# Performance work log

Hardware: AMD Instinct MI355X
Metric: run time of the kernel (lower is better)

## Reference

```python
import jax, jax.numpy as jnp
import numpy as np

N, D, K = 65536, 256, 4096
INIT_COUNT = 100  # torch: counts = ones(K, int32) * 100


def setup_inputs() -> dict:
    key = jax.random.key(0)
    k1, k2 = jax.random.split(key)
    embedded = jax.random.normal(k1, (N, D), dtype=jnp.float32)
    centers = jax.random.normal(k2, (K, D), dtype=jnp.float32)
    counts = jnp.full((K,), INIT_COUNT, dtype=jnp.int32)
    return {"embedded": embedded, "centers": centers, "counts": counts}


def reference(embedded, centers, counts):
    # --- predict_hard: squared euclidean distance [N,K] + argmin ---
    x2 = jnp.sum(embedded * embedded, axis=1, keepdims=True)       # [N,1]
    c2 = jnp.sum(centers * centers, axis=1)                        # [K]
    d2 = x2 - 2.0 * (embedded @ centers.T) + c2                    # [N,K]
    labels = jnp.argmin(d2, axis=1).astype(jnp.int32)              # [N]

    # --- dcn_loss: mean over batch of squared dist to assigned center ---
    loss = jnp.sum((embedded - centers[labels]) ** 2) / embedded.shape[0]

    # --- update_centroids: sequential running-mean update, closed form ---
    # c <- (1-1/n)c + (1/n)x repeated over assigned samples collapses to
    # (count0 * c0 + sum_assigned x) / (count0 + m)
    seg_sum = jax.ops.segment_sum(embedded, labels, num_segments=K)            # [K,D]
    seg_cnt = jax.ops.segment_sum(
        jnp.ones((embedded.shape[0],), dtype=embedded.dtype), labels, num_segments=K
    )                                                                           # [K]
    c0 = counts.astype(embedded.dtype)                                          # [K]
    new_centers = (c0[:, None] * centers + seg_sum) / (c0 + seg_cnt)[:, None]  # [K,D]
    new_counts = counts + seg_cnt.astype(jnp.int32)                             # [K]
    return labels, new_centers, new_counts, loss
```

## Files before the change

kernel.cpp:

```cpp
#include <hip/hip_runtime.h>
#include <cfloat>
#include <cstdint>

constexpr int N  = 65536;
constexpr int D  = 256;
constexpr int K  = 4096;

typedef __attribute__((ext_vector_type(8))) _Float16 half8;
typedef __attribute__((ext_vector_type(8))) unsigned short ushort8;
typedef __attribute__((ext_vector_type(4))) float floatx4;

__device__ __forceinline__ floatx4 mfma_f16(half8 a, half8 b, floatx4 c) {
    return __builtin_amdgcn_mfma_f32_16x16x32_f16(a, b, c, 0, 0, 0);
}

__device__ __forceinline__ void ld_lds16(void* lds, const void* g) {
    __builtin_amdgcn_global_load_lds(
        (const __attribute__((address_space(1))) unsigned int*)g,
        (__attribute__((address_space(3))) unsigned int*)lds, 16, 0, 0);
}

__global__ void prep_c2(const float* __restrict__ C, float* __restrict__ c2) {
    int k = blockIdx.x;
    int l = threadIdx.x;
    const float4* row = (const float4*)(C + (size_t)k * D);
    float4 v = row[l];
    float s = v.x*v.x + v.y*v.y + v.z*v.z + v.w*v.w;
    #pragma unroll
    for (int m = 1; m < 64; m <<= 1) s += __shfl_xor(s, m);
    if (l == 0) c2[k] = s;
}

__global__ void convert_f16_both(const float* __restrict__ X, const float* __restrict__ C,
                                 unsigned short* __restrict__ Xh,
                                 unsigned short* __restrict__ Ch,
                                 float* __restrict__ xsq_part,
                                 float* __restrict__ c2) {
    __shared__ float red[4];
    int id = blockIdx.x * 256 + threadIdx.x;
    const int nX = N * D / 8;
    bool isX = id < nX;
    const float* src; unsigned short* dst;
    if (isX) { src = X; dst = Xh; }
    else     { src = C; dst = Ch; id -= nX; }
    const float4* s4 = (const float4*)src;
    float4 a = s4[2*id], b = s4[2*id+1];
    float xs[8] = {a.x,a.y,a.z,a.w,b.x,b.y,b.z,b.w};
    ushort8 h;
    float ps = 0.f;
    #pragma unroll
    for (int i = 0; i < 8; ++i) {
        union { _Float16 f; unsigned short u; } cv;
        cv.f = (_Float16)xs[i];
        h[i] = cv.u;
        ps += xs[i]*xs[i];
    }
    ((ushort8*)dst)[id] = h;
    int t = threadIdx.x;
    if (isX) {
        #pragma unroll
        for (int m = 1; m < 64; m <<= 1) ps += __shfl_xor(ps, m);
        if ((t & 63) == 0) red[t >> 6] = ps;
        __syncthreads();
        if (t == 0) xsq_part[blockIdx.x] = (red[0] + red[1]) + (red[2] + red[3]);
    } else {
        #pragma unroll
        for (int m = 1; m < 32; m <<= 1) ps += __shfl_xor(ps, m);
        if ((t & 31) == 0) c2[id >> 5] = ps;
    }
}

__global__ __launch_bounds__(256, 2) void mfma_assign(
        const unsigned short* __restrict__ Xh, const unsigned short* __restrict__ Ch,
        const float* __restrict__ c2, float* __restrict__ cand)
{
    __shared__ __align__(16) unsigned short sA[8*128*4*8];
    __shared__ __align__(16) unsigned short sB[2*128*4*8];

    const int t    = threadIdx.x;
    const int w    = t >> 6, l = t & 63;
    const int quad = l >> 4, lr = l & 15;
    const int wm   = w >> 1, wn = w & 1;
    const int rowbase = blockIdx.x * 128;
    const int kb   = blockIdx.y;

    const int rl  = l >> 2;
    const int gsw = (l & 3) ^ ((l >> 3) & 3);

    #pragma unroll
    for (int k = 0; k < 2; ++k) {
        int q = 2*w + k;
        const unsigned short* gp = Ch + (size_t)(kb*1024 + q*16 + rl)*D + gsw*8;
        ld_lds16((char*)sB + q*1024, gp);
    }
    #pragma unroll
    for (int k = 0; k < 16; ++k) {
        int q = w*16 + k;
        int c = q >> 3, rb = (q & 7) * 16;
        const unsigned short* gp = Xh + (size_t)(rowbase + rb + rl)*D + c*32 + gsw*8;
        ld_lds16((char*)sA + q*1024, gp);
    }

    const unsigned short* gpB = Ch + (size_t)(kb*1024 + 2*w*16 + rl)*D + gsw*8 + 32;

    const int sA_off = ((64*wm + lr)*4 + (quad ^ ((lr>>1)&3)))*16;
    const int sB_off = ((64*wn + lr)*4 + (quad ^ ((lr>>1)&3)))*16;

    float v1[16], v2[16]; int x1[16], x2s[16];
    #pragma unroll
    for (int i = 0; i < 16; ++i) { v1[i]=FLT_MAX; v2[i]=FLT_MAX; x1[i]=0x7fffffff; x2s[i]=0x7fffffff; }

    floatx4 acc[4][4];
    float c2v[4]; int jidx[4];
    int buf = 0;

    for (int chunk = 0; chunk < 64; ++chunk) {
        const int dk = chunk & 7;
        const int ct = kb*8 + (chunk >> 3);

        if (dk == 0) {
            #pragma unroll
            for (int i = 0; i < 4; ++i)
                #pragma unroll
                for (int j = 0; j < 4; ++j) acc[i][j] = (floatx4)0.f;
            const int colbase = ct*128 + 64*wn;
            #pragma unroll
            for (int j = 0; j < 4; ++j) {
                int col = colbase + 16*j + lr;
                c2v[j] = c2[col]; jidx[j] = col;
            }
        }

        __syncthreads();

        if (chunk < 63) {
            int nc = chunk + 1;
            ld_lds16((char*)sB + (buf^1)*8192 + (2*w+0)*1024, gpB);
            ld_lds16((char*)sB + (buf^1)*8192 + (2*w+1)*1024, gpB + 16*D);
            gpB += ((nc & 7) == 7) ? (size_t)(128*D - 7*32) : 32;
        }

        half8 Af[4], Bf[4];
        #pragma unroll
        for (int i = 0; i < 4; ++i)
            Af[i] = *(const half8*)((const char*)sA + dk*8192 + i*1024 + sA_off);
        #pragma unroll
        for (int j = 0; j < 4; ++j)
            Bf[j] = *(const half8*)((const char*)sB + buf*8192 + j*1024 + sB_off);
        #pragma unroll
        for (int j = 0; j < 4; ++j)
            #pragma unroll
            for (int i = 0; i < 4; ++i)
                acc[i][j] = mfma_f16(Af[i], Bf[j], acc[i][j]);

        if (dk == 7) {
            #pragma unroll
            for (int i = 0; i < 4; ++i)
                #pragma unroll
                for (int j = 0; j < 4; ++j)
                    #pragma unroll
                    for (int r = 0; r < 4; ++r) {
                        float s = fmaf(-2.f, acc[i][j][r], c2v[j]);
                        int st = 4*i + r;
                        bool cA = s < v1[st];
                        bool cB = s < v2[st];
                        float tv = cB ? s : v2[st]; int tx = cB ? jidx[j] : x2s[st];
                        v2[st] = cA ? v1[st] : tv;  x2s[st] = cA ? x1[st] : tx;
                        v1[st] = cA ? s : v1[st];   x1[st]  = cA ? jidx[j] : x1[st];
                    }
        }
        buf ^= 1;
    }

    #pragma unroll
    for (int i = 0; i < 4; ++i)
        #pragma unroll
        for (int r = 0; r < 4; ++r) {
            int st = 4*i + r;
            float a1 = v1[st], a2 = v2[st]; int ax1 = x1[st], ax2 = x2s[st];
            #pragma unroll
            for (int m = 1; m < 16; m <<= 1) {
                float b1f = __shfl_xor(a1, m); int bx1 = __shfl_xor(ax1, m);
                float b2f = __shfl_xor(a2, m); int bx2 = __shfl_xor(ax2, m);
                bool tt = (b1f < a1) || (b1f == a1 && bx1 < ax1);
                float n1 = tt ? b1f : a1; int nx1 = tt ? bx1 : ax1;
                float w1 = tt ? a1 : b1f; int wx1 = tt ? ax1 : bx1;
                float w2 = tt ? b2f : a2; int wx2 = tt ? bx2 : ax2;
                bool uu = (w2 < w1) || (w2 == w1 && wx2 < wx1);
                a1 = n1; ax1 = nx1;
                a2 = uu ? w2 : w1; ax2 = uu ? wx2 : wx1;
            }
            if (lr == 0) {
                int row = rowbase + 64*wm + 16*i + 4*quad + r;
                float4 o; o.x = a1; o.y = __int_as_float(ax1);
                o.z = a2; o.w = __int_as_float(ax2);
                ((float4*)cand)[(size_t)row*8 + 2*kb + wn] = o;
            }
        }
}

__global__ __launch_bounds__(256) void recheck_label(
        const float* __restrict__ X, const float* __restrict__ C,
        const float* __restrict__ c2, const float* __restrict__ cand,
        float* __restrict__ out_labels, int* __restrict__ labInt,
        int* __restrict__ cnt)
{
    int t = threadIdx.x, w = t >> 6, l = t & 63;
    int g  = l >> 4;
    int lr = l & 15;
    int row0 = (blockIdx.x * 4 + w) * 4;
    int row  = row0 + g;

    float4 e = ((const float4*)cand)[(size_t)row*8 + (lr >> 1)];
    float s  = (lr & 1) ? e.z : e.x;
    int  idx = (lr & 1) ? __float_as_int(e.w) : __float_as_int(e.y);

    float a1 = s, a2 = FLT_MAX; int ax1 = idx, ax2 = 0x7fffffff;
    #pragma unroll
    for (int m = 1; m < 16; m <<= 1) {
        float b1 = __shfl_xor(a1, m); int bx1 = __shfl_xor(ax1, m);
        float b2 = __shfl_xor(a2, m); int bx2 = __shfl_xor(ax2, m);
        bool tt = (b1 < a1) || (b1 == a1 && bx1 < ax1);
        float n1 = tt ? b1 : a1; int nx1 = tt ? bx1 : ax1;
        float w1 = tt ? a1 : b1; int wx1 = tt ? ax1 : bx1;
        float w2 = tt ? b2 : a2; int wx2 = tt ? bx2 : ax2;
        bool uu = (w2 < w1) || (w2 == w1 && wx2 < wx1);
        a1 = n1; ax1 = nx1;
        a2 = uu ? w2 : w1; ax2 = uu ? wx2 : wx1;
    }

    bool certain = (a2 - a1 > 0.25f);
    unsigned long long certMask = __ballot(certain);

    if (certain && lr == 0) {
        out_labels[row] = (float)ax1;
        labInt[row] = ax1;
        atomicAdd(&cnt[ax1], 1);
    }

    #pragma unroll
    for (int q = 0; q < 4; ++q) {
        if ((certMask >> (q*16)) & 1ull) continue;
        int r = row0 + q;
        float sq  = __shfl(s,   q*16 + lr);
        int   iq  = __shfl(idx, q*16 + lr);
        float gs1 = __shfl(a1,  q*16);

        float4 xv = ((const float4*)X)[(size_t)r*64 + l];
        float px = xv.x*xv.x + xv.y*xv.y + xv.z*xv.z + xv.w*xv.w;
        #pragma unroll
        for (int m = 1; m < 64; m <<= 1) px += __shfl_xor(px, m);

        bool active = (l < 16) && (sq <= gs1 + 0.25f);
        unsigned long long mask = __ballot(active);
        float best = FLT_MAX; int bi = 0x7fffffff;
        while (mask) {
            int k = __ffsll((long long)mask) - 1;
            mask &= mask - 1;
            int ck = __shfl(iq, k);
            float4 cv = ((const float4*)C)[(size_t)ck*64 + l];
            float pd = xv.x*cv.x + xv.y*cv.y + xv.z*cv.z + xv.w*cv.w;
            #pragma unroll
            for (int m = 1; m < 64; m <<= 1) pd += __shfl_xor(pd, m);
            float d2 = fmaf(-2.f, pd, px) + c2[ck];
            if (d2 < best || (d2 == best && ck < bi)) { best = d2; bi = ck; }
        }
        if (l == 0) {
            out_labels[r] = (float)bi;
            labInt[r] = bi;
            atomicAdd(&cnt[bi], 1);
        }
    }
}

__global__ void prefix_kernel(const int* __restrict__ cnt,
                              int* __restrict__ offs, int* __restrict__ cursor) {
    int l = threadIdx.x;
    int s = 0;
    #pragma unroll 8
    for (int i = 0; i < 64; ++i) s += cnt[l*64 + i];
    int inc = s;
    #pragma unroll
    for (int off = 1; off < 64; off <<= 1) {
        int u = __shfl_up(inc, off);
        if (l >= off) inc += u;
    }
    int run = inc - s;
    for (int i = 0; i < 64; ++i) {
        int k = l*64 + i;
        offs[k] = run; cursor[k] = run;
        run += cnt[k];
    }
}

__global__ void scatter_idx(const int* __restrict__ labInt,
                            int* __restrict__ cursor, int* __restrict__ sortedIdx) {
    int i = blockIdx.x * 256 + threadIdx.x;
    int lab = labInt[i];
    int pos = atomicAdd(&cursor[lab], 1);
    sortedIdx[pos] = i;
}

__global__ __launch_bounds__(256) void center_update(
        const float* __restrict__ X, const float* __restrict__ C,
        const int* __restrict__ counts0, const int* __restrict__ cnt,
        const int* __restrict__ offs, const int* __restrict__ sortedIdx,
        float* __restrict__ lossC, float* __restrict__ out)
{
    __shared__ float red[4];
    int k = blockIdx.x, d = threadIdx.x;
    int start = offs[k], m = cnt[k];
    float acc = 0.f;
    int i = 0;
    for (; i + 4 <= m; i += 4) {
        int r0 = sortedIdx[start+i],   r1 = sortedIdx[start+i+1];
        int r2 = sortedIdx[start+i+2], r3 = sortedIdx[start+i+3];
        float a0 = X[(size_t)r0*D + d], a1 = X[(size_t)r1*D + d];
        float a2 = X[(size_t)r2*D + d], a3 = X[(size_t)r3*D + d];
        acc += (a0 + a1) + (a2 + a3);
    }
    for (; i < m; ++i) acc += X[(size_t)sortedIdx[start+i]*D + d];

    float cv = C[(size_t)k*D + d];
    float c0 = (float)counts0[k];
    out[N + (size_t)k*D + d] = (c0 * cv + acc) / (c0 + (float)m);
    if (d == 0) out[N + (size_t)K*D + k] = (float)(counts0[k] + m);

    float lp = cv * fmaf((float)m, cv, -2.f*acc);
    #pragma unroll
    for (int s = 1; s < 64; s <<= 1) lp += __shfl_xor(lp, s);
    if ((d & 63) == 0) red[d >> 6] = lp;
    __syncthreads();
    if (d == 0) lossC[k] = (red[0] + red[1]) + (red[2] + red[3]);
}

__global__ __launch_bounds__(256) void loss_final(
        const float* __restrict__ xsq_part, const float* __restrict__ lossC,
        float* __restrict__ out)
{
    __shared__ double red[4];
    int t = threadIdx.x;
    double s = 0.0;
    for (int i = t; i < 8192; i += 256) s += (double)xsq_part[i];
    for (int i = t; i < 4096; i += 256) s += (double)lossC[i];
    #pragma unroll
    for (int m = 1; m < 64; m <<= 1) s += __shfl_xor(s, m);
    if ((t & 63) == 0) red[t >> 6] = s;
    __syncthreads();
    if (t == 0)
        out[N + (size_t)K*D + K] = (float)(((red[0] + red[1]) + (red[2] + red[3])) / (double)N);
}

__global__ void finalize_kernel(const float* __restrict__ C,
                                const int* __restrict__ counts0,
                                const float* __restrict__ seg,
                                const int* __restrict__ cnt,
                                const double* __restrict__ lossAcc,
                                float* __restrict__ out)
{
    int g = blockIdx.x * 256 + threadIdx.x;
    int k = g >> 8;
    float c0 = (float)counts0[k];
    float m  = (float)cnt[k];
    out[N + g] = (c0 * C[g] + seg[g]) / (c0 + m);
    if (g < K) out[N + (size_t)K*D + g] = (float)(counts0[g] + cnt[g]);
    if (g == 0) out[N + (size_t)K*D + K] = (float)(lossAcc[0] / (double)N);
}

__global__ __launch_bounds__(256, 2) void assign_fp32(
        const float* __restrict__ X, const float* __restrict__ C,
        const float* __restrict__ c2, float* __restrict__ out_labels,
        float* __restrict__ seg, int* __restrict__ cnt,
        double* __restrict__ lossAcc)
{
    constexpr int BM = 128, BN = 128, KD = 16;
    __shared__ float As[KD][BM];
    __shared__ float Bs[KD][BN];
    __shared__ float x2f[BM];
    __shared__ int   labs[BM];

    const int t  = threadIdx.x;
    const int tx = t & 15;
    const int ty = t >> 4;
    const int rowbase = blockIdx.x * BM;

    {
        int r  = t >> 1;
        int dh = (t & 1) * (D / 2);
        const float4* xr = (const float4*)(X + (size_t)(rowbase + r) * D + dh);
        float s = 0.f;
        #pragma unroll
        for (int i = 0; i < D / 8; ++i) {
            float4 v = xr[i];
            s += v.x*v.x + v.y*v.y + v.z*v.z + v.w*v.w;
        }
        s += __shfl_xor(s, 1);
        if ((t & 1) == 0) x2f[r] = s;
    }
    __syncthreads();

    float x2v[8];
    #pragma unroll
    for (int i = 0; i < 4; ++i) { x2v[i] = x2f[4*ty + i]; x2v[i+4] = x2f[64 + 4*ty + i]; }

    float rmv[8]; int rmi[8];
    #pragma unroll
    for (int i = 0; i < 8; ++i) { rmv[i] = FLT_MAX; rmi[i] = 0x7fffffff; }

    for (int ct = 0; ct < K / BN; ++ct) {
        float acc[8][8];
        #pragma unroll
        for (int i = 0; i < 8; ++i)
            #pragma unroll
            for (int j = 0; j < 8; ++j) acc[i][j] = 0.f;

        float c2f2[8];
        {
            float4 a = *(const float4*)(c2 + ct*BN + 4*tx);
            float4 b = *(const float4*)(c2 + ct*BN + 64 + 4*tx);
            c2f2[0]=a.x; c2f2[1]=a.y; c2f2[2]=a.z; c2f2[3]=a.w;
            c2f2[4]=b.x; c2f2[5]=b.y; c2f2[6]=b.z; c2f2[7]=b.w;
        }

        for (int dk = 0; dk < D / KD; ++dk) {
            #pragma unroll
            for (int i = 0; i < 2; ++i) {
                int f  = t + 256 * i;
                int r  = f >> 2;
                int dp = f & 3;
                float4 av = *(const float4*)(X + (size_t)(rowbase + r) * D + dk*KD + 4*dp);
                float4 bv = *(const float4*)(C + (size_t)(ct*BN + r) * D + dk*KD + 4*dp);
                As[4*dp+0][r]=av.x; As[4*dp+1][r]=av.y; As[4*dp+2][r]=av.z; As[4*dp+3][r]=av.w;
                Bs[4*dp+0][r]=bv.x; Bs[4*dp+1][r]=bv.y; Bs[4*dp+2][r]=bv.z; Bs[4*dp+3][r]=bv.w;
            }
            __syncthreads();
            #pragma unroll
            for (int kk = 0; kk < KD; ++kk) {
                float4 a0 = *(const float4*)&As[kk][4*ty];
                float4 a1 = *(const float4*)&As[kk][64 + 4*ty];
                float4 b0 = *(const float4*)&Bs[kk][4*tx];
                float4 b1 = *(const float4*)&Bs[kk][64 + 4*tx];
                float av[8] = {a0.x,a0.y,a0.z,a0.w,a1.x,a1.y,a1.z,a1.w};
                float bv[8] = {b0.x,b0.y,b0.z,b0.w,b1.x,b1.y,b1.z,b1.w};
                #pragma unroll
                for (int i = 0; i < 8; ++i)
                    #pragma unroll
                    for (int j = 0; j < 8; ++j)
                        acc[i][j] = fmaf(av[i], bv[j], acc[i][j]);
            }
            __syncthreads();
        }

        #pragma unroll
        for (int i = 0; i < 8; ++i) {
            float bv = FLT_MAX; int bi = 0x7fffffff;
            #pragma unroll
            for (int j = 0; j < 8; ++j) {
                int coll = (j < 4) ? (4*tx + j) : (64 + 4*tx + (j - 4));
                float v = fmaf(-2.f, acc[i][j], x2v[i]) + c2f2[j];
                int idx = ct * BN + coll;
                if (v < bv || (v == bv && idx < bi)) { bv = v; bi = idx; }
            }
            #pragma unroll
            for (int m = 1; m < 16; m <<= 1) {
                float ov = __shfl_xor(bv, m);
                int   oi = __shfl_xor(bi, m);
                if (ov < bv || (ov == bv && oi < bi)) { bv = ov; bi = oi; }
            }
            if (bv < rmv[i] || (bv == rmv[i] && bi < rmi[i])) { rmv[i] = bv; rmi[i] = bi; }
        }
    }

    if (tx == 0) {
        #pragma unroll
        for (int i = 0; i < 8; ++i) {
            int r = (i < 4) ? (4*ty + i) : (64 + 4*ty + (i - 4));
            labs[r] = rmi[i];
            out_labels[rowbase + r] = (float)rmi[i];
            atomicAdd(&cnt[rmi[i]], 1);
        }
    }
    __syncthreads();

    {
        int r   = t >> 1;
        int dh  = (t & 1) * (D / 2);
        int lab = labs[r];
        const float4* xr = (const float4*)(X + (size_t)(rowbase + r) * D + dh);
        const float4* cr = (const float4*)(C + (size_t)lab * D + dh);
        float* sp = seg + (size_t)lab * D + dh;
        float ls = 0.f;
        #pragma unroll 8
        for (int i = 0; i < D / 8; ++i) {
            float4 xv = xr[i];
            float4 cv = cr[i];
            atomicAdd(sp + 4*i + 0, xv.x);
            atomicAdd(sp + 4*i + 1, xv.y);
            atomicAdd(sp + 4*i + 2, xv.z);
            atomicAdd(sp + 4*i + 3, xv.w);
            float d0 = xv.x - cv.x, d1 = xv.y - cv.y;
            float d2 = xv.z - cv.z, d3 = xv.w - cv.w;
            ls += d0*d0 + d1*d1 + d2*d2 + d3*d3;
        }
        #pragma unroll
        for (int m = 1; m < 64; m <<= 1) ls += __shfl_xor(ls, m);
        if ((t & 63) == 0) atomicAdd(lossAcc, (double)ls);
    }
}

extern "C" void kernel_launch(void* const* d_in, const int* in_sizes, int n_in,
                              void* d_out, int out_size, void* d_ws, size_t ws_size,
                              hipStream_t stream) {
    const float* X       = (const float*)d_in[0];
    const float* C       = (const float*)d_in[1];
    const int*   counts0 = (const int*)d_in[2];
    float* out = (float*)d_out;

    char* p = (char*)d_ws;
    float*  seg     = (float*)p;          p += (size_t)K * D * 4;
    int*    cnt     = (int*)p;            p += (size_t)K * 4;
    float*  c2      = (float*)p;          p += (size_t)K * 4;
    double* lossAcc = (double*)p;         p += 16;
    size_t zero_all = (size_t)(p - (char*)d_ws);
    float*  cand    = (float*)p;          p += (size_t)N * 32 * 4;
    unsigned short* Xh = (unsigned short*)p; p += (size_t)N * D * 2;
    unsigned short* Ch = (unsigned short*)p; p += (size_t)K * D * 2;
    float* xsq_part = (float*)p;          p += 8192 * 4;
    float* lossC    = (float*)p;          p += (size_t)K * 4;
    size_t need = (size_t)(p - (char*)d_ws);

    int* labInt    = (int*)seg;
    int* sortedIdx = labInt + N;
    int* offs      = sortedIdx + N;
    int* cursor    = offs + K;

    if (ws_size >= need) {
        hipMemsetAsync(cnt, 0, (size_t)K * 4, stream);
        convert_f16_both<<<(N*D/8 + K*D/8)/256, 256, 0, stream>>>(X, C, Xh, Ch, xsq_part, c2);
        mfma_assign<<<dim3(N/128, 4), 256, 0, stream>>>(Xh, Ch, c2, cand);
        recheck_label<<<N/16, 256, 0, stream>>>(X, C, c2, cand, out, labInt, cnt);
        prefix_kernel<<<1, 64, 0, stream>>>(cnt, offs, cursor);
        scatter_idx<<<N/256, 256, 0, stream>>>(labInt, cursor, sortedIdx);
        center_update<<<K, 256, 0, stream>>>(X, C, counts0, cnt, offs, sortedIdx, lossC, out);
        loss_final<<<1, 256, 0, stream>>>(xsq_part, lossC, out);
    } else {
        hipMemsetAsync(d_ws, 0, zero_all, stream);
        prep_c2<<<K, 64, 0, stream>>>(C, c2);
        assign_fp32<<<N/128, 256, 0, stream>>>(X, C, c2, out, seg, cnt, lossAcc);
        finalize_kernel<<<(K*D)/256, 256, 0, stream>>>(C, counts0, seg, cnt, lossAcc, out);
    }
}
```

Before: 572.2 us.

## Pre-swizzle centers into MFMA fragment layout and load B directly from global

The f16 conversion kernel now writes the center matrix in a layout that matches the MFMA B-fragment order, so each lane can load its half8 operands straight from global/L2. The assign kernel drops the LDS double-buffer for B and the per-chunk __syncthreads, and instead software-pipelines register double-buffers for both A (from LDS) and B (from global) across the 8 K-slices. This removes barrier and LDS staging overhead in the distance GEMM. The cost is that B is re-read from L2 by each wave without LDS sharing, plus higher register pressure.

```diff
diff --git a/kernel.cpp b/kernel.cpp
--- a/kernel.cpp
+++ b/kernel.cpp
@@ -33,16 +33,16 @@
 
 __global__ void convert_f16_both(const float* __restrict__ X, const float* __restrict__ C,
                                  unsigned short* __restrict__ Xh,
-                                 unsigned short* __restrict__ Ch,
+                                 unsigned short* __restrict__ Cf,
                                  float* __restrict__ xsq_part,
                                  float* __restrict__ c2) {
     __shared__ float red[4];
     int id = blockIdx.x * 256 + threadIdx.x;
     const int nX = N * D / 8;
     bool isX = id < nX;
-    const float* src; unsigned short* dst;
-    if (isX) { src = X; dst = Xh; }
-    else     { src = C; dst = Ch; id -= nX; }
+    const float* src;
+    if (isX) { src = X; }
+    else     { src = C; id -= nX; }
     const float4* s4 = (const float4*)src;
     float4 a = s4[2*id], b = s4[2*id+1];
     float xs[8] = {a.x,a.y,a.z,a.w,b.x,b.y,b.z,b.w};
@@ -55,27 +55,31 @@
         h[i] = cv.u;
         ps += xs[i]*xs[i];
     }
-    ((ushort8*)dst)[id] = h;
     int t = threadIdx.x;
     if (isX) {
+        ((ushort8*)Xh)[id] = h;
         #pragma unroll
         for (int m = 1; m < 64; m <<= 1) ps += __shfl_xor(ps, m);
         if ((t & 63) == 0) red[t >> 6] = ps;
         __syncthreads();
         if (t == 0) xsq_part[blockIdx.x] = (red[0] + red[1]) + (red[2] + red[3]);
     } else {
+        int c    = id >> 5;
+        int dk   = (id >> 2) & 7;
+        int quad = id & 3;
+        int flat = (((c >> 6) * 8 + dk) * 4 + ((c >> 4) & 3)) * 64 + quad * 16 + (c & 15);
+        ((ushort8*)Cf)[flat] = h;
         #pragma unroll
         for (int m = 1; m < 32; m <<= 1) ps += __shfl_xor(ps, m);
-        if ((t & 31) == 0) c2[id >> 5] = ps;
+        if ((t & 31) == 0) c2[c] = ps;
     }
 }
 
 __global__ __launch_bounds__(256, 2) void mfma_assign(
-        const unsigned short* __restrict__ Xh, const unsigned short* __restrict__ Ch,
+        const unsigned short* __restrict__ Xh, const unsigned short* __restrict__ Cfu,
         const float* __restrict__ c2, float* __restrict__ cand)
 {
     __shared__ __align__(16) unsigned short sA[8*128*4*8];
-    __shared__ __align__(16) unsigned short sB[2*128*4*8];
 
     const int t    = threadIdx.x;
     const int w    = t >> 6, l = t & 63;
@@ -88,12 +92,6 @@
     const int gsw = (l & 3) ^ ((l >> 3) & 3);
 
     #pragma unroll
-    for (int k = 0; k < 2; ++k) {
-        int q = 2*w + k;
-        const unsigned short* gp = Ch + (size_t)(kb*1024 + q*16 + rl)*D + gsw*8;
-        ld_lds16((char*)sB + q*1024, gp);
-    }
-    #pragma unroll
     for (int k = 0; k < 16; ++k) {
         int q = w*16 + k;
         int c = q >> 3, rb = (q & 7) * 16;
@@ -101,10 +99,32 @@
         ld_lds16((char*)sA + q*1024, gp);
     }
 
-    const unsigned short* gpB = Ch + (size_t)(kb*1024 + 2*w*16 + rl)*D + gsw*8 + 32;
-
+    const half8* pB = (const half8*)Cfu + (size_t)(kb*16 + wn)*2048 + l;
+    const char* sAc = (const char*)sA;
     const int sA_off = ((64*wm + lr)*4 + (quad ^ ((lr>>1)&3)))*16;
-    const int sB_off = ((64*wn + lr)*4 + (quad ^ ((lr>>1)&3)))*16;
+
+    half8 A0[4], A1[4], B0[4], B1[4];
+
+#define LOADB(Bs, bump) do {                                            \
+        Bs[0] = pB[0]; Bs[1] = pB[64]; Bs[2] = pB[128]; Bs[3] = pB[192]; \
+        pB += (bump); } while (0)
+
+#define LOADA(As, dkn) do {                                             \
+        As[0] = *(const half8*)(sAc + ((dkn)*8192 + 0*1024) + sA_off);  \
+        As[1] = *(const half8*)(sAc + ((dkn)*8192 + 1*1024) + sA_off);  \
+        As[2] = *(const half8*)(sAc + ((dkn)*8192 + 2*1024) + sA_off);  \
+        As[3] = *(const half8*)(sAc + ((dkn)*8192 + 3*1024) + sA_off); } while (0)
+
+#define MF16(As, Bs) do {                                               \
+        _Pragma("unroll")                                               \
+        for (int j_ = 0; j_ < 4; ++j_)                                  \
+            _Pragma("unroll")                                           \
+            for (int i_ = 0; i_ < 4; ++i_)                              \
+                acc[i_][j_] = mfma_f16(As[i_], Bs[j_], acc[i_][j_]); } while (0)
+
+    LOADB(B0, 256);
+    __syncthreads();
+    LOADA(A0, 0);
 
     float v1[16], v2[16]; int x1[16], x2s[16];
     #pragma unroll
@@ -112,65 +132,47 @@
 
     floatx4 acc[4][4];
     float c2v[4]; int jidx[4];
-    int buf = 0;
-
-    for (int chunk = 0; chunk < 64; ++chunk) {
-        const int dk = chunk & 7;
-        const int ct = kb*8 + (chunk >> 3);
-
-        if (dk == 0) {
-            #pragma unroll
-            for (int i = 0; i < 4; ++i)
+
+    for (int e = 0; e < 8; ++e) {
+        #pragma unroll
+        for (int i = 0; i < 4; ++i)
+            #pragma unroll
+            for (int j = 0; j < 4; ++j) acc[i][j] = (floatx4)0.f;
+        const int colbase = (kb*8 + e)*128 + 64*wn;
+        #pragma unroll
+        for (int j = 0; j < 4; ++j) {
+            int col = colbase + 16*j + lr;
+            c2v[j] = c2[col]; jidx[j] = col;
+        }
+
+        LOADB(B1, 256);  LOADA(A1, 1); MF16(A0, B0);
+        LOADB(B0, 256);  LOADA(A0, 2); MF16(A1, B1);
+        LOADB(B1, 256);  LOADA(A1, 3); MF16(A0, B0);
+        LOADB(B0, 256);  LOADA(A0, 4); MF16(A1, B1);
+        LOADB(B1, 256);  LOADA(A1, 5); MF16(A0, B0);
+        LOADB(B0, 256);  LOADA(A0, 6); MF16(A1, B1);
+        LOADB(B1, 2304); LOADA(A1, 7); MF16(A0, B0);
+        LOADB(B0, 256);  LOADA(A0, 0); MF16(A1, B1);
+
+        #pragma unroll
+        for (int i = 0; i < 4; ++i)
+            #pragma unroll
+            for (int j = 0; j < 4; ++j)
                 #pragma unroll
-                for (int j = 0; j < 4; ++j) acc[i][j] = (floatx4)0.f;
-            const int colbase = ct*128 + 64*wn;
-            #pragma unroll
-            for (int j = 0; j < 4; ++j) {
-                int col = colbase + 16*j + lr;
-                c2v[j] = c2[col]; jidx[j] = col;
-            }
-        }
-
-        __syncthreads();
-
-        if (chunk < 63) {
-            int nc = chunk + 1;
-            ld_lds16((char*)sB + (buf^1)*8192 + (2*w+0)*1024, gpB);
-            ld_lds16((char*)sB + (buf^1)*8192 + (2*w+1)*1024, gpB + 16*D);
-            gpB += ((nc & 7) == 7) ? (size_t)(128*D - 7*32) : 32;
-        }
-
-        half8 Af[4], Bf[4];
-        #pragma unroll
-        for (int i = 0; i < 4; ++i)
-            Af[i] = *(const half8*)((const char*)sA + dk*8192 + i*1024 + sA_off);
-        #pragma unroll
-        for (int j = 0; j < 4; ++j)
-            Bf[j] = *(const half8*)((const char*)sB + buf*8192 + j*1024 + sB_off);
-        #pragma unroll
-        for (int j = 0; j < 4; ++j)
-            #pragma unroll
-            for (int i = 0; i < 4; ++i)
-                acc[i][j] = mfma_f16(Af[i], Bf[j], acc[i][j]);
-
-        if (dk == 7) {
-            #pragma unroll
-            for (int i = 0; i < 4; ++i)
-                #pragma unroll
-                for (int j = 0; j < 4; ++j)
-                    #pragma unroll
-                    for (int r = 0; r < 4; ++r) {
-                        float s = fmaf(-2.f, acc[i][j][r], c2v[j]);
-                        int st = 4*i + r;
-                        bool cA = s < v1[st];
-                        bool cB = s < v2[st];
-                        float tv = cB ? s : v2[st]; int tx = cB ? jidx[j] : x2s[st];
-                        v2[st] = cA ? v1[st] : tv;  x2s[st] = cA ? x1[st] : tx;
-                        v1[st] = cA ? s : v1[st];   x1[st]  = cA ? jidx[j] : x1[st];
-                    }
-        }
-        buf ^= 1;
-    }
+                for (int r = 0; r < 4; ++r) {
+                    float s = fmaf(-2.f, acc[i][j][r], c2v[j]);
+                    int st = 4*i + r;
+                    bool cA = s < v1[st];
+                    bool cB = s < v2[st];
+                    float tv = cB ? s : v2[st]; int tx = cB ? jidx[j] : x2s[st];
+                    v2[st] = cA ? v1[st] : tv;  x2s[st] = cA ? x1[st] : tx;
+                    v1[st] = cA ? s : v1[st];   x1[st]  = cA ? jidx[j] : x1[st];
+                }
+    }
+
+#undef LOADB
+#undef LOADA
+#undef MF16
 
     #pragma unroll
     for (int i = 0; i < 4; ++i)
@@ -524,7 +526,7 @@
     size_t zero_all = (size_t)(p - (char*)d_ws);
     float*  cand    = (float*)p;          p += (size_t)N * 32 * 4;
     unsigned short* Xh = (unsigned short*)p; p += (size_t)N * D * 2;
-    unsigned short* Ch = (unsigned short*)p; p += (size_t)K * D * 2;
+    unsigned short* Cf = (unsigned short*)p; p += (size_t)K * D * 2;
     float* xsq_part = (float*)p;          p += 8192 * 4;
     float* lossC    = (float*)p;          p += (size_t)K * 4;
     size_t need = (size_t)(p - (char*)d_ws);
@@ -536,8 +538,8 @@
 
     if (ws_size >= need) {
         hipMemsetAsync(cnt, 0, (size_t)K * 4, stream);
-        convert_f16_both<<<(N*D/8 + K*D/8)/256, 256, 0, stream>>>(X, C, Xh, Ch, xsq_part, c2);
-        mfma_assign<<<dim3(N/128, 4), 256, 0, stream>>>(Xh, Ch, c2, cand);
+        convert_f16_both<<<(N*D/8 + K*D/8)/256, 256, 0, stream>>>(X, C, Xh, Cf, xsq_part, c2);
+        mfma_assign<<<dim3(N/128, 4), 256, 0, stream>>>(Xh, Cf, c2, cand);
         recheck_label<<<N/16, 256, 0, stream>>>(X, C, c2, cand, out, labInt, cnt);
         prefix_kernel<<<1, 64, 0, stream>>>(cnt, offs, cursor);
         scatter_idx<<<N/256, 256, 0, stream>>>(labInt, cursor, sortedIdx);
```

After: 626.4 us. +9.5%, slower.

## Restructure MFMA assign kernel: double-buffer A and B, narrower wave tiles, occupancy 3

Applied to the files above, without the earlier changes.

The distance-GEMM kernel no longer keeps the whole 128x256 X tile resident in LDS. It streams A and B together in 64-wide K slices through double buffers, and each wave now owns 32 rows by 64 columns instead of 64 by 64. Center norms are staged once into shared memory, and the per-thread top-2 state is halved, with a flush midway. The goals are lower LDS and register use, so the launch bound can rise to 3 blocks per CU, and better overlap of loads with MFMA. In exchange, each MFMA now needs more LDS fragment loads and more X is loaded per block, which could lower arithmetic intensity.

```diff
diff --git a/kernel.cpp b/kernel.cpp
--- a/kernel.cpp
+++ b/kernel.cpp
@@ -70,92 +70,130 @@
     }
 }
 
-__global__ __launch_bounds__(256, 2) void mfma_assign(
+__global__ __launch_bounds__(256, 3) void mfma_assign(
         const unsigned short* __restrict__ Xh, const unsigned short* __restrict__ Ch,
-        const float* __restrict__ c2, float* __restrict__ cand)
+        const float* __restrict__ c2g, float* __restrict__ cand)
 {
-    __shared__ __align__(16) unsigned short sA[8*128*4*8];
-    __shared__ __align__(16) unsigned short sB[2*128*4*8];
+    __shared__ __align__(16) unsigned short sA[2*8192];
+    __shared__ __align__(16) unsigned short sB[2*4096];
+    __shared__ float sC2[1024];
 
     const int t    = threadIdx.x;
     const int w    = t >> 6, l = t & 63;
     const int quad = l >> 4, lr = l & 15;
-    const int wm   = w >> 1, wn = w & 1;
     const int rowbase = blockIdx.x * 128;
     const int kb   = blockIdx.y;
 
     const int rl  = l >> 2;
     const int gsw = (l & 3) ^ ((l >> 3) & 3);
 
-    #pragma unroll
-    for (int k = 0; k < 2; ++k) {
-        int q = 2*w + k;
-        const unsigned short* gp = Ch + (size_t)(kb*1024 + q*16 + rl)*D + gsw*8;
-        ld_lds16((char*)sB + q*1024, gp);
-    }
-    #pragma unroll
-    for (int k = 0; k < 16; ++k) {
-        int q = w*16 + k;
-        int c = q >> 3, rb = (q & 7) * 16;
-        const unsigned short* gp = Xh + (size_t)(rowbase + rb + rl)*D + c*32 + gsw*8;
-        ld_lds16((char*)sA + q*1024, gp);
-    }
-
-    const unsigned short* gpB = Ch + (size_t)(kb*1024 + 2*w*16 + rl)*D + gsw*8 + 32;
-
-    const int sA_off = ((64*wm + lr)*4 + (quad ^ ((lr>>1)&3)))*16;
-    const int sB_off = ((64*wn + lr)*4 + (quad ^ ((lr>>1)&3)))*16;
-
-    float v1[16], v2[16]; int x1[16], x2s[16];
-    #pragma unroll
-    for (int i = 0; i < 16; ++i) { v1[i]=FLT_MAX; v2[i]=FLT_MAX; x1[i]=0x7fffffff; x2s[i]=0x7fffffff; }
-
-    floatx4 acc[4][4];
+    ((float4*)sC2)[t] = ((const float4*)(c2g + kb*1024))[t];
+
+#define STAGE(nk, db) do {                                                     \
+        _Pragma("unroll")                                                      \
+        for (int m_ = 0; m_ < 4; ++m_) {                                       \
+            int dkk_ = m_ & 1, q_ = 2*w + (m_ >> 1);                           \
+            const unsigned short* gp_ = Xh + (size_t)(rowbase + q_*16 + rl)*D  \
+                + (((nk) & 3)*2 + dkk_)*32 + gsw*8;                            \
+            ld_lds16((char*)sA + (db)*16384 + dkk_*8192 + q_*1024, gp_);       \
+        }                                                                      \
+        _Pragma("unroll")                                                      \
+        for (int dkk_ = 0; dkk_ < 2; ++dkk_) {                                 \
+            const unsigned short* gp_ = Ch + (size_t)(kb*1024 + ((nk)>>2)*64   \
+                + w*16 + rl)*D + (((nk) & 3)*2 + dkk_)*32 + gsw*8;             \
+            ld_lds16((char*)sB + (db)*8192 + dkk_*4096 + w*1024, gp_);         \
+        }                                                                      \
+    } while (0)
+
+    STAGE(0, 0);
+
+    const char* sAc = (const char*)sA;
+    const char* sBc = (const char*)sB;
+    const int slot   = quad ^ ((lr >> 1) & 3);
+    const int sA_off = ((32*w + lr)*4 + slot)*16;
+    const int sB_off = (lr*4 + slot)*16;
+
+#define KSTEP(dkk) do {                                                        \
+        const char* aB_ = sAc + buf*16384 + (dkk)*8192;                        \
+        const char* bB_ = sBc + buf*8192  + (dkk)*4096;                        \
+        half8 Af0 = *(const half8*)(aB_ + 0*1024 + sA_off);                    \
+        half8 Af1 = *(const half8*)(aB_ + 1*1024 + sA_off);                    \
+        half8 Bf0 = *(const half8*)(bB_ + 0*1024 + sB_off);                    \
+        half8 Bf1 = *(const half8*)(bB_ + 1*1024 + sB_off);                    \
+        half8 Bf2 = *(const half8*)(bB_ + 2*1024 + sB_off);                    \
+        half8 Bf3 = *(const half8*)(bB_ + 3*1024 + sB_off);                    \
+        acc[0][0] = mfma_f16(Af0, Bf0, acc[0][0]);                             \
+        acc[1][0] = mfma_f16(Af1, Bf0, acc[1][0]);                             \
+        acc[0][1] = mfma_f16(Af0, Bf1, acc[0][1]);                             \
+        acc[1][1] = mfma_f16(Af1, Bf1, acc[1][1]);                             \
+        acc[0][2] = mfma_f16(Af0, Bf2, acc[0][2]);                             \
+        acc[1][2] = mfma_f16(Af1, Bf2, acc[1][2]);                             \
+        acc[0][3] = mfma_f16(Af0, Bf3, acc[0][3]);                             \
+        acc[1][3] = mfma_f16(Af1, Bf3, acc[1][3]);                             \
+    } while (0)
+
+#define FLUSH(h) do {                                                          \
+    _Pragma("unroll")                                                          \
+    for (int i = 0; i < 2; ++i)                                                \
+        _Pragma("unroll")                                                      \
+        for (int r = 0; r < 4; ++r) {                                          \
+            int st = 4*i + r;                                                  \
+            float a1 = v1[st], a2 = v2[st]; int ax1 = x1[st], ax2 = x2s[st];   \
+            _Pragma("unroll")                                                  \
+            for (int m = 1; m < 16; m <<= 1) {                                 \
+                float b1f = __shfl_xor(a1, m); int bx1 = __shfl_xor(ax1, m);   \
+                float b2f = __shfl_xor(a2, m); int bx2 = __shfl_xor(ax2, m);   \
+                bool tt = (b1f < a1) || (b1f == a1 && bx1 < ax1);              \
+                float n1 = tt ? b1f : a1; int nx1 = tt ? bx1 : ax1;            \
+                float w1 = tt ? a1 : b1f; int wx1 = tt ? ax1 : bx1;            \
+                float w2 = tt ? b2f : a2; int wx2 = tt ? bx2 : ax2;            \
+                bool uu = (w2 < w1) || (w2 == w1 && wx2 < wx1);                \
+                a1 = n1; ax1 = nx1;                                            \
+                a2 = uu ? w2 : w1; ax2 = uu ? wx2 : wx1;                       \
+            }                                                                  \
+            if (lr == 0) {                                                     \
+                int row = rowbase + 32*w + 16*i + 4*quad + r;                  \
+                float4 o; o.x = a1; o.y = __int_as_float(ax1);                 \
+                o.z = a2; o.w = __int_as_float(ax2);                           \
+                ((float4*)cand)[(size_t)row*8 + (h)] = o;                      \
+            }                                                                  \
+            v1[st] = FLT_MAX; v2[st] = FLT_MAX;                                \
+            x1[st] = 0x7fffffff; x2s[st] = 0x7fffffff;                         \
+        } } while (0)
+
+    float v1[8], v2[8]; int x1[8], x2s[8];
+    #pragma unroll
+    for (int i = 0; i < 8; ++i) { v1[i]=FLT_MAX; v2[i]=FLT_MAX; x1[i]=0x7fffffff; x2s[i]=0x7fffffff; }
+
+    floatx4 acc[2][4];
     float c2v[4]; int jidx[4];
     int buf = 0;
 
-    for (int chunk = 0; chunk < 64; ++chunk) {
-        const int dk = chunk & 7;
-        const int ct = kb*8 + (chunk >> 3);
-
-        if (dk == 0) {
-            #pragma unroll
-            for (int i = 0; i < 4; ++i)
+    for (int ks = 0; ks < 64; ++ks) {
+        __syncthreads();
+
+        if (ks < 63) STAGE(ks + 1, buf ^ 1);
+
+        if ((ks & 3) == 0) {
+            const int ct = ks >> 2;
+            #pragma unroll
+            for (int i = 0; i < 2; ++i)
                 #pragma unroll
                 for (int j = 0; j < 4; ++j) acc[i][j] = (floatx4)0.f;
-            const int colbase = ct*128 + 64*wn;
             #pragma unroll
             for (int j = 0; j < 4; ++j) {
-                int col = colbase + 16*j + lr;
-                c2v[j] = c2[col]; jidx[j] = col;
+                int cc = ct*64 + 16*j + lr;
+                c2v[j] = sC2[cc];
+                jidx[j] = kb*1024 + cc;
             }
         }
 
-        __syncthreads();
-
-        if (chunk < 63) {
-            int nc = chunk + 1;
-            ld_lds16((char*)sB + (buf^1)*8192 + (2*w+0)*1024, gpB);
-            ld_lds16((char*)sB + (buf^1)*8192 + (2*w+1)*1024, gpB + 16*D);
-            gpB += ((nc & 7) == 7) ? (size_t)(128*D - 7*32) : 32;
-        }
-
-        half8 Af[4], Bf[4];
-        #pragma unroll
-        for (int i = 0; i < 4; ++i)
-            Af[i] = *(const half8*)((const char*)sA + dk*8192 + i*1024 + sA_off);
-        #pragma unroll
-        for (int j = 0; j < 4; ++j)
-            Bf[j] = *(const half8*)((const char*)sB + buf*8192 + j*1024 + sB_off);
-        #pragma unroll
-        for (int j = 0; j < 4; ++j)
-            #pragma unroll
-            for (int i = 0; i < 4; ++i)
-                acc[i][j] = mfma_f16(Af[i], Bf[j], acc[i][j]);
-
-        if (dk == 7) {
-            #pragma unroll
-            for (int i = 0; i < 4; ++i)
+        KSTEP(0);
+        KSTEP(1);
+
+        if ((ks & 3) == 3) {
+            #pragma unroll
+            for (int i = 0; i < 2; ++i)
                 #pragma unroll
                 for (int j = 0; j < 4; ++j)
                     #pragma unroll
@@ -169,34 +207,14 @@
                         v1[st] = cA ? s : v1[st];   x1[st]  = cA ? jidx[j] : x1[st];
                     }
         }
+        if (ks == 31) FLUSH(2*kb);
         buf ^= 1;
     }
-
-    #pragma unroll
-    for (int i = 0; i < 4; ++i)
-        #pragma unroll
-        for (int r = 0; r < 4; ++r) {
-            int st = 4*i + r;
-            float a1 = v1[st], a2 = v2[st]; int ax1 = x1[st], ax2 = x2s[st];
-            #pragma unroll
-            for (int m = 1; m < 16; m <<= 1) {
-                float b1f = __shfl_xor(a1, m); int bx1 = __shfl_xor(ax1, m);
-                float b2f = __shfl_xor(a2, m); int bx2 = __shfl_xor(ax2, m);
-                bool tt = (b1f < a1) || (b1f == a1 && bx1 < ax1);
-                float n1 = tt ? b1f : a1; int nx1 = tt ? bx1 : ax1;
-                float w1 = tt ? a1 : b1f; int wx1 = tt ? ax1 : bx1;
-                float w2 = tt ? b2f : a2; int wx2 = tt ? bx2 : ax2;
-                bool uu = (w2 < w1) || (w2 == w1 && wx2 < wx1);
-                a1 = n1; ax1 = nx1;
-                a2 = uu ? w2 : w1; ax2 = uu ? wx2 : wx1;
-            }
-            if (lr == 0) {
-                int row = rowbase + 64*wm + 16*i + 4*quad + r;
-                float4 o; o.x = a1; o.y = __int_as_float(ax1);
-                o.z = a2; o.w = __int_as_float(ax2);
-                ((float4*)cand)[(size_t)row*8 + 2*kb + wn] = o;
-            }
-        }
+    FLUSH(2*kb + 1);
+
+#undef STAGE
+#undef KSTEP
+#undef FLUSH
 }
 
 __global__ __launch_bounds__(256) void recheck_label(
```

After: 651.9 us. 1.14x slower.

## Restructure MFMA assign kernel with 4-stage streamed A/B pipeline and swizzled grid

Applied to the files above, without the earlier changes.

The distance/argmin kernel no longer keeps the whole 128-row X tile resident in LDS. It now streams both X and C chunks through a 4-deep LDS ring using async global-to-LDS loads with explicit vmcnt waits. Each block covers 128 rows by 512 centers and a 1D grid with a swizzled block index, each wave owns 32 rows by 64 columns, c2 is staged in LDS, and occupancy is raised to 3 blocks per CU. The aim is to hide memory latency and improve L2 reuse of X panels across neighbouring blocks. The trade-off is that X is reloaded once per center tile, and the smaller per-wave tile lowers MFMA reuse per LDS read.

```diff
diff --git a/kernel.cpp b/kernel.cpp
--- a/kernel.cpp
+++ b/kernel.cpp
@@ -70,110 +70,124 @@
     }
 }
 
-__global__ __launch_bounds__(256, 2) void mfma_assign(
+__global__ __launch_bounds__(256, 3) void mfma_assign(
         const unsigned short* __restrict__ Xh, const unsigned short* __restrict__ Ch,
-        const float* __restrict__ c2, float* __restrict__ cand)
+        const float* __restrict__ c2g, float* __restrict__ cand)
 {
-    __shared__ __align__(16) unsigned short sA[8*128*4*8];
-    __shared__ __align__(16) unsigned short sB[2*128*4*8];
+    __shared__ __align__(16) unsigned short sBuf[4 * 6144];
+    __shared__ float sC2[512];
 
     const int t    = threadIdx.x;
     const int w    = t >> 6, l = t & 63;
     const int quad = l >> 4, lr = l & 15;
-    const int wm   = w >> 1, wn = w & 1;
-    const int rowbase = blockIdx.x * 128;
-    const int kb   = blockIdx.y;
+
+    const int bid   = blockIdx.x;
+    const int sw    = (bid & 7) * 512 + (bid >> 3);
+    const int kb8   = sw & 7;
+    const int panel = sw >> 3;
+    const int rowbase = panel * 128;
 
     const int rl  = l >> 2;
     const int gsw = (l & 3) ^ ((l >> 3) & 3);
 
-    #pragma unroll
-    for (int k = 0; k < 2; ++k) {
-        int q = 2*w + k;
-        const unsigned short* gp = Ch + (size_t)(kb*1024 + q*16 + rl)*D + gsw*8;
-        ld_lds16((char*)sB + q*1024, gp);
-    }
-    #pragma unroll
-    for (int k = 0; k < 16; ++k) {
-        int q = w*16 + k;
-        int c = q >> 3, rb = (q & 7) * 16;
-        const unsigned short* gp = Xh + (size_t)(rowbase + rb + rl)*D + c*32 + gsw*8;
-        ld_lds16((char*)sA + q*1024, gp);
-    }
-
-    const unsigned short* gpB = Ch + (size_t)(kb*1024 + 2*w*16 + rl)*D + gsw*8 + 32;
-
-    const int sA_off = ((64*wm + lr)*4 + (quad ^ ((lr>>1)&3)))*16;
-    const int sB_off = ((64*wn + lr)*4 + (quad ^ ((lr>>1)&3)))*16;
-
-    float v1[16], v2[16]; int x1[16], x2s[16];
-    #pragma unroll
-    for (int i = 0; i < 16; ++i) { v1[i]=FLT_MAX; v2[i]=FLT_MAX; x1[i]=0x7fffffff; x2s[i]=0x7fffffff; }
-
-    floatx4 acc[4][4];
+    if (t < 128) ((float4*)sC2)[t] = ((const float4*)(c2g + kb8*512))[t];
+    asm volatile("s_waitcnt vmcnt(0) lgkmcnt(0)" ::: "memory");
+
+    const unsigned short* pA0 = Xh + (size_t)(rowbase + 2*w*16 + rl)*D + gsw*8;
+    const unsigned short* pA1 = pA0 + (size_t)16*D;
+    const unsigned short* pB  = Ch + (size_t)(kb8*512 + w*16 + rl)*D + gsw*8;
+
+#define ISSUE(db) do {                                                         \
+        ld_lds16((char*)sBuf + (db)*12288 + (2*w+0)*1024, pA0);                \
+        ld_lds16((char*)sBuf + (db)*12288 + (2*w+1)*1024, pA1);                \
+        ld_lds16((char*)sBuf + (db)*12288 + 8192 + w*1024, pB);                \
+    } while (0)
+#define ADV(big) do {                                                          \
+        if (big) { pA0 -= 224; pA1 -= 224; pB += 16160; }                      \
+        else     { pA0 += 32;  pA1 += 32;  pB += 32;    }                      \
+    } while (0)
+
+    ISSUE(0); ADV(false);
+    ISSUE(1); ADV(false);
+    ISSUE(2); ADV(false);
+
+    const char* sAc = (const char*)sBuf;
+    const int slot   = quad ^ ((lr >> 1) & 3);
+    const int sA_off = ((32*w + lr)*4 + slot)*16;
+    const int sB_off = (lr*4 + slot)*16;
+
+    float v1[8], v2[8]; int x1[8], x2s[8];
+    #pragma unroll
+    for (int i = 0; i < 8; ++i) { v1[i]=FLT_MAX; v2[i]=FLT_MAX; x1[i]=0x7fffffff; x2s[i]=0x7fffffff; }
+
+    floatx4 acc[2][4];
     float c2v[4]; int jidx[4];
-    int buf = 0;
-
-    for (int chunk = 0; chunk < 64; ++chunk) {
-        const int dk = chunk & 7;
-        const int ct = kb*8 + (chunk >> 3);
-
-        if (dk == 0) {
-            #pragma unroll
-            for (int i = 0; i < 4; ++i)
+
+    for (int ct = 0; ct < 8; ++ct) {
+        #pragma unroll
+        for (int s = 0; s < 8; ++s) {
+            asm volatile("s_waitcnt vmcnt(6) lgkmcnt(0)" ::: "memory");
+            __builtin_amdgcn_s_barrier();
+            __builtin_amdgcn_sched_barrier(0);
+            ISSUE((s + 3) & 3);
+            ADV(s == 4);
+
+            if (s == 0) {
                 #pragma unroll
-                for (int j = 0; j < 4; ++j) acc[i][j] = (floatx4)0.f;
-            const int colbase = ct*128 + 64*wn;
-            #pragma unroll
-            for (int j = 0; j < 4; ++j) {
-                int col = colbase + 16*j + lr;
-                c2v[j] = c2[col]; jidx[j] = col;
-            }
-        }
-
-        __syncthreads();
-
-        if (chunk < 63) {
-            int nc = chunk + 1;
-            ld_lds16((char*)sB + (buf^1)*8192 + (2*w+0)*1024, gpB);
-            ld_lds16((char*)sB + (buf^1)*8192 + (2*w+1)*1024, gpB + 16*D);
-            gpB += ((nc & 7) == 7) ? (size_t)(128*D - 7*32) : 32;
-        }
-
-        half8 Af[4], Bf[4];
-        #pragma unroll
-        for (int i = 0; i < 4; ++i)
-            Af[i] = *(const half8*)((const char*)sA + dk*8192 + i*1024 + sA_off);
-        #pragma unroll
-        for (int j = 0; j < 4; ++j)
-            Bf[j] = *(const half8*)((const char*)sB + buf*8192 + j*1024 + sB_off);
-        #pragma unroll
-        for (int j = 0; j < 4; ++j)
-            #pragma unroll
-            for (int i = 0; i < 4; ++i)
-                acc[i][j] = mfma_f16(Af[i], Bf[j], acc[i][j]);
-
-        if (dk == 7) {
-            #pragma unroll
-            for (int i = 0; i < 4; ++i)
+                for (int i = 0; i < 2; ++i)
+                    #pragma unroll
+                    for (int j = 0; j < 4; ++j) acc[i][j] = (floatx4)0.f;
                 #pragma unroll
-                for (int j = 0; j < 4; ++j)
+                for (int j = 0; j < 4; ++j) {
+                    int cc = ct*64 + 16*j + lr;
+                    c2v[j] = sC2[cc];
+                    jidx[j] = kb8*512 + cc;
+                }
+            }
+
+            {
+                const char* aB_ = sAc + (s & 3)*12288;
+                const char* bB_ = aB_ + 8192;
+                half8 Af0 = *(const half8*)(aB_ + 0*1024 + sA_off);
+                half8 Af1 = *(const half8*)(aB_ + 1*1024 + sA_off);
+                half8 Bf0 = *(const half8*)(bB_ + 0*1024 + sB_off);
+                half8 Bf1 = *(const half8*)(bB_ + 1*1024 + sB_off);
+                half8 Bf2 = *(const half8*)(bB_ + 2*1024 + sB_off);
+                half8 Bf3 = *(const half8*)(bB_ + 3*1024 + sB_off);
+                acc[0][0] = mfma_f16(Af0, Bf0, acc[0][0]);
+                acc[1][0] = mfma_f16(Af1, Bf0, acc[1][0]);
+                acc[0][1] = mfma_f16(Af0, Bf1, acc[0][1]);
+                acc[1][1] = mfma_f16(Af1, Bf1, acc[1][1]);
+                acc[0][2] = mfma_f16(Af0, Bf2, acc[0][2]);
+                acc[1][2] = mfma_f16(Af1, Bf2, acc[1][2]);
+                acc[0][3] = mfma_f16(Af0, Bf3, acc[0][3]);
+                acc[1][3] = mfma_f16(Af1, Bf3, acc[1][3]);
+            }
+
+            if (s == 7) {
+                #pragma unroll
+                for (int i = 0; i < 2; ++i)
                     #pragma unroll
-                    for (int r = 0; r < 4; ++r) {
-                        float s = fmaf(-2.f, acc[i][j][r], c2v[j]);
-                        int st = 4*i + r;
-                        bool cA = s < v1[st];
-                        bool cB = s < v2[st];
-                        float tv = cB ? s : v2[st]; int tx = cB ? jidx[j] : x2s[st];
-                        v2[st] = cA ? v1[st] : tv;  x2s[st] = cA ? x1[st] : tx;
-                        v1[st] = cA ? s : v1[st];   x1[st]  = cA ? jidx[j] : x1[st];
-                    }
-        }
-        buf ^= 1;
-    }
-
-    #pragma unroll
-    for (int i = 0; i < 4; ++i)
+                    for (int j = 0; j < 4; ++j)
+                        #pragma unroll
+                        for (int r = 0; r < 4; ++r) {
+                            float sc = fmaf(-2.f, acc[i][j][r], c2v[j]);
+                            int st = 4*i + r;
+                            bool cA = sc < v1[st];
+                            bool cB = sc < v2[st];
+                            float tv = cB ? sc : v2[st]; int tx = cB ? jidx[j] : x2s[st];
+                            v2[st] = cA ? v1[st] : tv;  x2s[st] = cA ? x1[st] : tx;
+                            v1[st] = cA ? sc : v1[st];  x1[st]  = cA ? jidx[j] : x1[st];
+                        }
+            }
+        }
+    }
+
+#undef ISSUE
+#undef ADV
+
+    #pragma unroll
+    for (int i = 0; i < 2; ++i)
         #pragma unroll
         for (int r = 0; r < 4; ++r) {
             int st = 4*i + r;
@@ -191,10 +205,10 @@
                 a2 = uu ? w2 : w1; ax2 = uu ? wx2 : wx1;
             }
             if (lr == 0) {
-                int row = rowbase + 64*wm + 16*i + 4*quad + r;
+                int row = rowbase + 32*w + 16*i + 4*quad + r;
                 float4 o; o.x = a1; o.y = __int_as_float(ax1);
                 o.z = a2; o.w = __int_as_float(ax2);
-                ((float4*)cand)[(size_t)row*8 + 2*kb + wn] = o;
+                ((float4*)cand)[(size_t)row*8 + kb8] = o;
             }
         }
 }
@@ -537,7 +551,7 @@
     if (ws_size >= need) {
         hipMemsetAsync(cnt, 0, (size_t)K * 4, stream);
         convert_f16_both<<<(N*D/8 + K*D/8)/256, 256, 0, stream>>>(X, C, Xh, Ch, xsq_part, c2);
-        mfma_assign<<<dim3(N/128, 4), 256, 0, stream>>>(Xh, Ch, c2, cand);
+        mfma_assign<<<4096, 256, 0, stream>>>(Xh, Ch, c2, cand);
         recheck_label<<<N/16, 256, 0, stream>>>(X, C, c2, cand, out, labInt, cnt);
         prefix_kernel<<<1, 64, 0, stream>>>(cnt, offs, cursor);
         scatter_idx<<<N/256, 256, 0, stream>>>(labInt, cursor, sortedIdx);
```

Result: slower. 645.8 us (+12.9%).
